# Performance work log

Measured on AMD Instinct MI355X. Metric: run time of the kernel, lower is better.

Reference implementation:

```python
import jax, jax.numpy as jnp
import numpy as np

SUPPORT = 10
NEIGHBOR_NUM = 20
DEGREE = 8
NEG_SLOPE = 0.2
EPS = 1e-12


def _norm(x, axis):
    n = jnp.linalg.norm(x, axis=axis, keepdims=True)
    return x / jnp.maximum(n, EPS)


def knn_index(v, k):
    # v: (b, n, 3) -> (b, n, k) indices of k nearest (self excluded)
    inner = jnp.einsum('bnd,bmd->bnm', v, v)
    quad = jnp.sum(v * v, axis=2)
    dist = quad[:, :, None] - 2.0 * inner + quad[:, None, :]
    _, idx = jax.lax.top_k(-dist, k + 1)  # smallest distances
    return idx[:, :, 1:]


def gather_nb(feat, idx):
    # feat (b,n,c), idx (b,n,k) -> (b,n,k,c)
    b = feat.shape[0]
    return feat[jnp.arange(b)[:, None, None], idx]


def nb_dir_norm(vertices, idx):
    nb = gather_nb(vertices, idx) - vertices[:, :, None, :]
    return _norm(nb, axis=-1)


def op3d(idx, vertices, directions, kernel_num):
    # Conv_surface: directions (3, support*kernel)
    ndn = nb_dir_norm(vertices, idx)                 # (b,n,k,3)
    sdn = _norm(directions, axis=0)
    theta = jax.nn.relu(jnp.einsum('bnkd,de->bnke', ndn, sdn))
    b, n, kk, _ = theta.shape
    theta = theta.reshape(b, n, kk, SUPPORT, kernel_num)
    return jnp.sum(jnp.max(theta, axis=2), axis=2)    # (b,n,kernel)


def opnd(idx, vertices, feat, w, bias, directions, out_ch):
    # Conv_layer: w (in,(s+1)*out), bias ((s+1)*out), directions (3, s*out)
    ndn = nb_dir_norm(vertices, idx)
    sdn = _norm(directions, axis=0)
    theta = jax.nn.relu(jnp.einsum('bnkd,de->bnke', ndn, sdn))  # (b,n,k,s*out)
    fo = feat @ w + bias                                        # (b,n,(s+1)*out)
    fc = fo[:, :, :out_ch]
    fs = gather_nb(fo[:, :, out_ch:], idx)                      # (b,n,k,s*out)
    b, n, kk, _ = theta.shape
    act = (theta * fs).reshape(b, n, kk, SUPPORT, out_ch)
    return fc + jnp.sum(jnp.max(act, axis=2), axis=2)


def tree_gcn(x, w_root, w_branch, w_l1, w_l2, bias, activation):
    # depth-0 upsampling TreeGCN: x (b,node,in) -> (b,node*DEGREE,out)
    b, node, in_f = x.shape
    root = x @ w_root                                           # (b,node,out)
    br = jax.nn.leaky_relu(jnp.einsum('bni,nij->bnj', x, w_branch), NEG_SLOPE)
    br = br.reshape(b, node * DEGREE, in_f)
    br = (br @ w_l1) @ w_l2                                     # (b,node*deg,out)
    out = jnp.repeat(root, DEGREE, axis=1) + br
    if activation:
        out = jax.nn.leaky_relu(out + jnp.tile(bias, (1, node, 1)), NEG_SLOPE)
    return out


def setup_inputs() -> dict:
    key = jax.random.key(0)
    ks = iter(jax.random.split(key, 32))
    r = lambda shape: (jax.random.normal(next(ks), shape, dtype=jnp.float32) * 0.1)
    inp = {
        'coase_points': jax.random.normal(next(ks), (2, 512, 3), dtype=jnp.float32),
        'd0': r((3, SUPPORT * 32)),
        'w1': r((32, (SUPPORT + 1) * 64)), 'b1': r(((SUPPORT + 1) * 64,)), 'dir1': r((3, SUPPORT * 64)),
        'd2': r((3, SUPPORT * 32)),
        'w3': r((32, (SUPPORT + 1) * 64)), 'b3': r(((SUPPORT + 1) * 64,)), 'dir3': r((3, SUPPORT * 64)),
        'w4': r((64, (SUPPORT + 1) * 64)), 'b4': r(((SUPPORT + 1) * 64,)), 'dir4': r((3, SUPPORT * 64)),
        'w5': r((64, (SUPPORT + 1) * 64)), 'b5': r(((SUPPORT + 1) * 64,)), 'dir5': r((3, SUPPORT * 64)),
        'root1': r((64, 3)), 'branch1': r((512, 64, DEGREE * 64)),
        'loop1a': r((64, 64 * SUPPORT)), 'loop1b': r((64 * SUPPORT, 3)), 'bias1': r((1, DEGREE, 3)),
        'root2': r((64, 3)), 'branch2': r((4096, 64, DEGREE * 64)),
        'loop2a': r((64, 64 * SUPPORT)), 'loop2b': r((64 * SUPPORT, 3)),
    }
    return inp


def reference(coase_points, d0, w1, b1, dir1, d2, w3, b3, dir3, w4, b4, dir4,
              w5, b5, dir5, root1, branch1, loop1a, loop1b, bias1,
              root2, branch2, loop2a, loop2b):
    idx = knn_index(coase_points, NEIGHBOR_NUM)
    fm0 = jax.nn.relu(op3d(idx, coase_points, d0, 32))  # dropout is identity in eval
    fm1 = jax.nn.relu(opnd(idx, coase_points, fm0, w1, b1, dir1, 64))
    pc1 = tree_gcn(fm1, root1, branch1, loop1a, loop1b, bias1, True)   # (b, 4096, 3)
    idx2 = knn_index(pc1, NEIGHBOR_NUM)
    fm2 = jax.nn.relu(op3d(idx2, pc1, d2, 32))
    fm3 = jax.nn.relu(opnd(idx2, pc1, fm2, w3, b3, dir3, 64))
    fm4 = jax.nn.relu(opnd(idx2, pc1, fm3, w4, b4, dir4, 64))
    fm5 = jax.nn.relu(opnd(idx2, pc1, fm4, w5, b5, dir5, 64))
    pc2 = tree_gcn(fm5, root2, branch2, loop2a, loop2b, None, False)   # (b, 32768, 3)
    return pc1, pc2
```

## Files before the change

kernel.cpp:

```cpp
#include <hip/hip_runtime.h>
#include <hip/hip_bf16.h>
#include <stdint.h>

#define SUPPORT 10
#define KNN 20
#define DEGREE 8

__global__ __launch_bounds__(256) void prep_kernel(
    const float* __restrict__ d0, const float* __restrict__ dir1,
    const float* __restrict__ d2, const float* __restrict__ dir3,
    const float* __restrict__ dir4, const float* __restrict__ dir5,
    float* __restrict__ sdn0, float* __restrict__ sdn1, float* __restrict__ sdn2,
    float* __restrict__ sdn3, float* __restrict__ sdn4, float* __restrict__ sdn5,
    const float* __restrict__ l1a, const float* __restrict__ l1b,
    const float* __restrict__ l2a, const float* __restrict__ l2b,
    float* __restrict__ wc1, float* __restrict__ wc2,
    const float* __restrict__ pts1,
    float* __restrict__ px1, float* __restrict__ py1, float* __restrict__ pz1) {
#pragma clang fp contract(off)
  if (blockIdx.x < 13) {
    int t = blockIdx.x * 256 + threadIdx.x;
    if (t >= 3200) return;
    const float* src; float* dst; int cols; int e;
    if (t < 320)       { src = d0;   dst = sdn0; cols = 320; e = t; }
    else if (t < 960)  { src = dir1; dst = sdn1; cols = 640; e = t - 320; }
    else if (t < 1280) { src = d2;   dst = sdn2; cols = 320; e = t - 960; }
    else if (t < 1920) { src = dir3; dst = sdn3; cols = 640; e = t - 1280; }
    else if (t < 2560) { src = dir4; dst = sdn4; cols = 640; e = t - 1920; }
    else               { src = dir5; dst = sdn5; cols = 640; e = t - 2560; }
    float a = src[e], b = src[cols + e], c = src[2 * cols + e];
    float nrm = sqrtf(a * a + b * b + c * c);
    nrm = fmaxf(nrm, 1e-12f);
    dst[e] = a / nrm; dst[cols + e] = b / nrm; dst[2 * cols + e] = c / nrm;
  } else if (blockIdx.x < 15) {
    int which = blockIdx.x - 13;
    int tt = threadIdx.x;
    if (tt >= 192) return;
    const float* A  = which ? l2a : l1a;
    const float* Bm = which ? l2b : l1b;
    float* out = which ? wc2 : wc1;
    int i = tt / 3, c = tt % 3;
    float s = 0.f;
    for (int k = 0; k < 640; ++k) s = fmaf(A[i * 640 + k], Bm[k * 3 + c], s);
    out[i * 3 + c] = s;
  } else {
    int t = (blockIdx.x - 15) * 256 + threadIdx.x;
    if (t >= 1024) return;
    px1[t] = pts1[t * 3];
    py1[t] = pts1[t * 3 + 1];
    pz1[t] = pts1[t * 3 + 2];
  }
}

template <int MPER, int WAVES>
__global__ __launch_bounds__(WAVES * 64) void knn_kernel(
    const float* __restrict__ px, const float* __restrict__ py,
    const float* __restrict__ pz, int N, int* __restrict__ idx_out,
    float* __restrict__ ndn) {
#pragma clang fp contract(off)
  extern __shared__ uint32_t kbuf[];
  int w = threadIdx.x >> 6, lane = threadIdx.x & 63;
  int g = blockIdx.x * WAVES + w;
  int b = g / N, n = g % N;
  volatile uint32_t* K = kbuf + (size_t)w * 64 * MPER;
  const float* PX = px + (size_t)b * N;
  const float* PY = py + (size_t)b * N;
  const float* PZ = pz + (size_t)b * N;

  float nx = PX[n], ny = PY[n], nz = PZ[n];
  float qn = nx * nx + ny * ny + nz * nz;

  unsigned long long mymin = ~0ull;
  for (int j = 0; j < MPER; ++j) {
    int m = j * 64 + lane;
    float mx = PX[m], my = PY[m], mz = PZ[m];
    float inner = nx * mx + ny * my + nz * mz;
    float qm = mx * mx + my * my + mz * mz;
    float d = (qn - 2.0f * inner) + qm;
    uint32_t u = __float_as_uint(d);
    u ^= (u & 0x80000000u) ? 0xFFFFFFFFu : 0x80000000u;
    K[lane * MPER + (j ^ (lane & (MPER - 1)))] = u;
    unsigned long long key = ((unsigned long long)u << 32) | (unsigned)m;
    mymin = key < mymin ? key : mymin;
  }
  unsigned pick = 0;
  for (int r = 0; r < 21; ++r) {
    unsigned long long best = mymin;
#pragma unroll
    for (int s = 1; s < 64; s <<= 1) {
      unsigned long long o = __shfl_xor(best, s, 64);
      best = o < best ? o : best;
    }
    unsigned m = (unsigned)best;
    if (r > 0 && lane == r - 1) pick = m;
    if (r == 20) break;
    int owner = m & 63, slot = m >> 6;
    if (lane == slot) K[owner * MPER + (slot ^ (owner & (MPER - 1)))] = 0xFFFFFFFFu;
    unsigned long long cand = ~0ull;
    if (lane < MPER) {
      uint32_t v = K[owner * MPER + (lane ^ (owner & (MPER - 1)))];
      cand = ((unsigned long long)v << 32) | (unsigned)(lane * 64 + owner);
    }
#pragma unroll
    for (int s = 1; s < 64; s <<= 1) {
      unsigned long long o = __shfl_xor(cand, s, 64);
      cand = o < cand ? o : cand;
    }
    if (lane == owner) mymin = cand;
  }
  if (lane < KNN) {
    idx_out[(size_t)g * KNN + lane] = (int)pick;
    float mx = PX[pick], my = PY[pick], mz = PZ[pick];
    float dx = mx - nx, dy = my - ny, dz = mz - nz;
    float nr = sqrtf(dx * dx + dy * dy + dz * dz);
    nr = fmaxf(nr, 1e-12f);
    size_t base = (size_t)g * 60 + (size_t)lane * 3;
    ndn[base] = dx / nr; ndn[base + 1] = dy / nr; ndn[base + 2] = dz / nr;
  }
}

__global__ __launch_bounds__(256) void op3dfo_kernel(const float* __restrict__ ndn,
                                                     const float* __restrict__ sdn,
                                                     const float* __restrict__ wmat,
                                                     const float* __restrict__ bias,
                                                     float* __restrict__ fo, int N) {
#pragma clang fp contract(off)
  __shared__ float ndL[8 * 60];
  __shared__ float fL[8 * 32];
  int t = threadIdx.x;
  int gbase = blockIdx.x * 8;
  for (int i = t; i < 8 * 60; i += 256) ndL[i] = ndn[(size_t)gbase * 60 + i];
  __syncthreads();
  {
    int gg = t >> 5, c = t & 31;
    const float* nd = ndL + gg * 60;
    float sv0[SUPPORT], sv1[SUPPORT], sv2[SUPPORT], mm[SUPPORT];
#pragma unroll
    for (int s = 0; s < SUPPORT; ++s) {
      sv0[s] = sdn[s * 32 + c];
      sv1[s] = sdn[320 + s * 32 + c];
      sv2[s] = sdn[640 + s * 32 + c];
      mm[s] = 0.f;
    }
    for (int k = 0; k < KNN; ++k) {
      float nx = nd[k * 3], ny = nd[k * 3 + 1], nz = nd[k * 3 + 2];
#pragma unroll
      for (int s = 0; s < SUPPORT; ++s) {
        float th = nx * sv0[s] + ny * sv1[s] + nz * sv2[s];
        mm[s] = fmaxf(mm[s], th);
      }
    }
    float acc = 0.f;
#pragma unroll
    for (int s = 0; s < SUPPORT; ++s) acc += mm[s];
    fL[gg * 32 + c] = acc;
  }
  __syncthreads();
  float a0[8], a1[8], a2[8];
#pragma unroll
  for (int gg = 0; gg < 8; ++gg) { a0[gg] = 0.f; a1[gg] = 0.f; a2[gg] = 0.f; }
  bool has3 = (t < 192);
  for (int i = 0; i < 32; ++i) {
    float w0 = wmat[i * 704 + t];
    float w1 = wmat[i * 704 + t + 256];
    float w2 = has3 ? wmat[i * 704 + t + 512] : 0.f;
#pragma unroll
    for (int gg = 0; gg < 8; ++gg) {
      float f = fL[gg * 32 + i];
      a0[gg] = fmaf(f, w0, a0[gg]);
      a1[gg] = fmaf(f, w1, a1[gg]);
      a2[gg] = fmaf(f, w2, a2[gg]);
    }
  }
  float b0 = bias[t], b1 = bias[t + 256], b2 = has3 ? bias[t + 512] : 0.f;
#pragma unroll
  for (int gg = 0; gg < 8; ++gg) {
    size_t base = (size_t)(gbase + gg) * 704;
    fo[base + t] = a0[gg] + b0;
    fo[base + t + 256] = a1[gg] + b1;
    if (has3) fo[base + t + 512] = a2[gg] + b2;
  }
}

__global__ __launch_bounds__(256) void fo_kernel(const float* __restrict__ feat,
                                                 const float* __restrict__ wmat,
                                                 const float* __restrict__ bias,
                                                 float* __restrict__ fo, int N) {
  __shared__ float fL[8 * 64];
  int t = threadIdx.x;
  int gbase = blockIdx.x * 8;
  for (int i = t; i < 8 * 64; i += 256) fL[i] = feat[(size_t)gbase * 64 + i];
  __syncthreads();
  float a0[8], a1[8], a2[8];
#pragma unroll
  for (int gg = 0; gg < 8; ++gg) { a0[gg] = 0.f; a1[gg] = 0.f; a2[gg] = 0.f; }
  bool has3 = (t < 192);
  for (int i = 0; i < 64; ++i) {
    float w0 = wmat[i * 704 + t];
    float w1 = wmat[i * 704 + t + 256];
    float w2 = has3 ? wmat[i * 704 + t + 512] : 0.f;
#pragma unroll
    for (int gg = 0; gg < 8; ++gg) {
      float f = fL[gg * 64 + i];
      a0[gg] = fmaf(f, w0, a0[gg]);
      a1[gg] = fmaf(f, w1, a1[gg]);
      a2[gg] = fmaf(f, w2, a2[gg]);
    }
  }
  float b0 = bias[t], b1 = bias[t + 256], b2 = has3 ? bias[t + 512] : 0.f;
#pragma unroll
  for (int gg = 0; gg < 8; ++gg) {
    size_t base = (size_t)(gbase + gg) * 704;
    fo[base + t] = a0[gg] + b0;
    fo[base + t + 256] = a1[gg] + b1;
    if (has3) fo[base + t + 512] = a2[gg] + b2;
  }
}

__global__ __launch_bounds__(256) void opnd_kernel(const float* __restrict__ ndn,
                                                   const int* __restrict__ idx,
                                                   const float* __restrict__ fo,
                                                   const float* __restrict__ sdn,
                                                   float* __restrict__ fm, int N) {
#pragma clang fp contract(off)
  __shared__ float ndL[4][64];
  __shared__ int offL[4][24];
  int nb = gridDim.x;
  int lb = (blockIdx.x & 7) * (nb >> 3) + (blockIdx.x >> 3);
  int w = threadIdx.x >> 6, lane = threadIdx.x & 63;
  int g = lb * 4 + w;
  if (lane < 60) ndL[w][lane] = ndn[(size_t)g * 60 + lane];
  if (lane < KNN) offL[w][lane] = ((g / N) * N + idx[(size_t)g * KNN + lane]) * 704 + 64;
  __syncthreads();
  const float* ndw = ndL[w];
  const int* offw = offL[w];
  float sv0[SUPPORT], sv1[SUPPORT], sv2[SUPPORT], mm[SUPPORT];
#pragma unroll
  for (int s = 0; s < SUPPORT; ++s) {
    sv0[s] = sdn[s * 64 + lane];
    sv1[s] = sdn[640 + s * 64 + lane];
    sv2[s] = sdn[1280 + s * 64 + lane];
    mm[s] = -__builtin_inff();
  }
  for (int k = 0; k < KNN; ++k) {
    float nx = ndw[k * 3], ny = ndw[k * 3 + 1], nz = ndw[k * 3 + 2];
    int off = offw[k];
#pragma unroll
    for (int s = 0; s < SUPPORT; ++s) {
      float t = fmaxf(nx * sv0[s] + ny * sv1[s] + nz * sv2[s], 0.f);
      float f = fo[(size_t)off + s * 64 + lane];
      mm[s] = fmaxf(mm[s], t * f);
    }
  }
  float acc = 0.f;
#pragma unroll
  for (int s = 0; s < SUPPORT; ++s) acc += mm[s];
  float fc = fo[(size_t)g * 704 + lane];
  float v = fc + acc;
  fm[(size_t)g * 64 + lane] = fmaxf(v, 0.f);
}

__global__ __launch_bounds__(256) void tree_exact_kernel(
    const float* __restrict__ x, const float* __restrict__ wroot,
    const float* __restrict__ wb, const float* __restrict__ l1,
    const float* __restrict__ l2, const float* __restrict__ bias,
    float* __restrict__ out, int node,
    float* __restrict__ px2, float* __restrict__ py2, float* __restrict__ pz2) {
#pragma clang fp contract(off)
  __shared__ float xL[2][64];
  __shared__ float brL[2][512];
  __shared__ float tL[16][640];
  __shared__ float rootv[2][3];
  int n = blockIdx.x, t = threadIdx.x;
  if (t < 128) xL[t >> 6][t & 63] = x[(size_t)(t >> 6) * node * 64 + (size_t)n * 64 + (t & 63)];
  __syncthreads();
  {
    const float* wrow = wb + (size_t)n * 64 * 512;
    int j0 = 2 * t;
    float a00 = 0.f, a01 = 0.f, a10 = 0.f, a11 = 0.f;
    for (int i = 0; i < 64; ++i) {
      float w0 = wrow[(size_t)i * 512 + j0];
      float w1 = wrow[(size_t)i * 512 + j0 + 1];
      float f0 = xL[0][i], f1 = xL[1][i];
      a00 = a00 + f0 * w0; a01 = a01 + f0 * w1;
      a10 = a10 + f1 * w0; a11 = a11 + f1 * w1;
    }
    brL[0][j0]     = a00 >= 0.f ? a00 : 0.2f * a00;
    brL[0][j0 + 1] = a01 >= 0.f ? a01 : 0.2f * a01;
    brL[1][j0]     = a10 >= 0.f ? a10 : 0.2f * a10;
    brL[1][j0 + 1] = a11 >= 0.f ? a11 : 0.2f * a11;
  }
  if (t < 6) {
    int b = t / 3, c = t % 3;
    float r = 0.f;
    for (int i = 0; i < 64; ++i) r = fmaf(xL[b][i], wroot[i * 3 + c], r);
    rootv[b][c] = r;
  }
  __syncthreads();
#pragma unroll 4
  for (int u = 0; u < 40; ++u) {
    int e = u * 256 + t;
    int p = e / 640, j = e % 640;
    const float* brow = brL[p >> 3] + (p & 7) * 64;
    float acc = 0.f;
    for (int i = 0; i < 64; ++i)
      acc = fmaf(brow[i], l1[i * 640 + j], acc);
    tL[p][j] = acc;
  }
  __syncthreads();
  if (t < 48) {
    int p = t / 3, c = t % 3, b = p >> 3, d = p & 7;
    float s = 0.f;
    for (int j = 0; j < 640; ++j) s = fmaf(tL[p][j], l2[j * 3 + c], s);
    float v = rootv[b][c] + s;
    v = v + bias[d * 3 + c];
    v = v >= 0.f ? v : 0.2f * v;
    out[((size_t)b * node * DEGREE + (size_t)n * DEGREE + d) * 3 + c] = v;
    int p2 = b * node * DEGREE + n * DEGREE + d;
    if (c == 0) px2[p2] = v; else if (c == 1) py2[p2] = v; else pz2[p2] = v;
  }
}

__global__ __launch_bounds__(256) void tree_kernel(const float* __restrict__ x,
                                                   const float* __restrict__ wroot,
                                                   const float* __restrict__ wb,
                                                   const float* __restrict__ wc,
                                                   float* __restrict__ out,
                                                   int node) {
  __shared__ float xL[2][2][64];
  __shared__ float brL[2][2][512];
  int t = threadIdx.x;
  int n0 = blockIdx.x * 2;
  {
    int which = t >> 6;
    int ns = which >> 1, bb = which & 1;
    xL[ns][bb][t & 63] = x[(size_t)bb * node * 64 + (size_t)(n0 + ns) * 64 + (t & 63)];
  }
  __syncthreads();
  int ns = t >> 7;
  int j0 = (t & 127) * 4;
  const float* wrow = wb + (size_t)(n0 + ns) * 64 * 512;
  float a0x = 0.f, a0y = 0.f, a0z = 0.f, a0w = 0.f;
  float a1x = 0.f, a1y = 0.f, a1z = 0.f, a1w = 0.f;
  for (int i = 0; i < 64; ++i) {
    float4 wv = *(const float4*)(wrow + (size_t)i * 512 + j0);
    float f0 = xL[ns][0][i], f1 = xL[ns][1][i];
    a0x += f0 * wv.x; a0y += f0 * wv.y; a0z += f0 * wv.z; a0w += f0 * wv.w;
    a1x += f1 * wv.x; a1y += f1 * wv.y; a1z += f1 * wv.z; a1w += f1 * wv.w;
  }
  brL[ns][0][j0]     = a0x >= 0.f ? a0x : 0.2f * a0x;
  brL[ns][0][j0 + 1] = a0y >= 0.f ? a0y : 0.2f * a0y;
  brL[ns][0][j0 + 2] = a0z >= 0.f ? a0z : 0.2f * a0z;
  brL[ns][0][j0 + 3] = a0w >= 0.f ? a0w : 0.2f * a0w;
  brL[ns][1][j0]     = a1x >= 0.f ? a1x : 0.2f * a1x;
  brL[ns][1][j0 + 1] = a1y >= 0.f ? a1y : 0.2f * a1y;
  brL[ns][1][j0 + 2] = a1z >= 0.f ? a1z : 0.2f * a1z;
  brL[ns][1][j0 + 3] = a1w >= 0.f ? a1w : 0.2f * a1w;
  __syncthreads();
  if (t < 96) {
    int nsub = t / 48, rem = t % 48;
    int b = rem / 24, r2 = rem % 24, d = r2 / 3, c = r2 % 3;
    float root = 0.f, brs = 0.f;
    for (int i = 0; i < 64; ++i) {
      root = fmaf(xL[nsub][b][i], wroot[i * 3 + c], root);
      brs  = fmaf(brL[nsub][b][d * 64 + i], wc[i * 3 + c], brs);
    }
    float v = root + brs;
    out[((size_t)b * node * DEGREE + (size_t)(n0 + nsub) * DEGREE + d) * 3 + c] = v;
  }
}

extern "C" void kernel_launch(void* const* d_in, const int* in_sizes, int n_in,
                              void* d_out, int out_size, void* d_ws, size_t ws_size,
                              hipStream_t stream) {
  const float* pts1    = (const float*)d_in[0];
  const float* d0      = (const float*)d_in[1];
  const float* w1      = (const float*)d_in[2];
  const float* b1      = (const float*)d_in[3];
  const float* dir1    = (const float*)d_in[4];
  const float* d2      = (const float*)d_in[5];
  const float* w3      = (const float*)d_in[6];
  const float* b3      = (const float*)d_in[7];
  const float* dir3    = (const float*)d_in[8];
  const float* w4      = (const float*)d_in[9];
  const float* b4      = (const float*)d_in[10];
  const float* dir4    = (const float*)d_in[11];
  const float* w5      = (const float*)d_in[12];
  const float* b5      = (const float*)d_in[13];
  const float* dir5    = (const float*)d_in[14];
  const float* root1   = (const float*)d_in[15];
  const float* branch1 = (const float*)d_in[16];
  const float* l1a     = (const float*)d_in[17];
  const float* l1b     = (const float*)d_in[18];
  const float* bias1   = (const float*)d_in[19];
  const float* root2   = (const float*)d_in[20];
  const float* branch2 = (const float*)d_in[21];
  const float* l2a     = (const float*)d_in[22];
  const float* l2b     = (const float*)d_in[23];

  float* ws = (float*)d_ws;
  size_t o = 0;
  float* sdn0 = ws + o; o += 960;
  float* sdn1 = ws + o; o += 1920;
  float* sdn2 = ws + o; o += 960;
  float* sdn3 = ws + o; o += 1920;
  float* sdn4 = ws + o; o += 1920;
  float* sdn5 = ws + o; o += 1920;
  float* wc1  = ws + o; o += 192;
  float* wc2  = ws + o; o += 192;
  float* px1  = ws + o; o += 1024;
  float* py1  = ws + o; o += 1024;
  float* pz1  = ws + o; o += 1024;
  float* px2  = ws + o; o += 8192;
  float* py2  = ws + o; o += 8192;
  float* pz2  = ws + o; o += 8192;
  int*   idxb = (int*)(ws + o); o += (size_t)2 * 4096 * KNN;
  float* ndnb = ws + o; o += (size_t)2 * 4096 * KNN * 3;
  float* fo   = ws + o; o += (size_t)2 * 4096 * 704;
  float* fmA  = ws + o; o += (size_t)2 * 4096 * 64;
  float* fmB  = ws + o; o += (size_t)2 * 4096 * 64;

  float* pc1 = (float*)d_out;
  float* pc2 = (float*)d_out + 2 * 4096 * 3;

  prep_kernel<<<19, 256, 0, stream>>>(d0, dir1, d2, dir3, dir4, dir5,
                                      sdn0, sdn1, sdn2, sdn3, sdn4, sdn5,
                                      l1a, l1b, l2a, l2b, wc1, wc2,
                                      pts1, px1, py1, pz1);

  knn_kernel<8, 4><<<2 * 512 / 4, 256, 4 * 64 * 8 * 4, stream>>>(px1, py1, pz1, 512, idxb, ndnb);
  op3dfo_kernel<<<2 * 512 / 8, 256, 0, stream>>>(ndnb, sdn0, w1, b1, fo, 512);
  opnd_kernel<<<2 * 512 / 4, 256, 0, stream>>>(ndnb, idxb, fo, sdn1, fmB, 512);
  tree_exact_kernel<<<512, 256, 0, stream>>>(fmB, root1, branch1, l1a, l1b,
                                             bias1, pc1, 512, px2, py2, pz2);

  knn_kernel<64, 2><<<2 * 4096 / 2, 128, 2 * 64 * 64 * 4, stream>>>(px2, py2, pz2, 4096, idxb, ndnb);
  op3dfo_kernel<<<2 * 4096 / 8, 256, 0, stream>>>(ndnb, sdn2, w3, b3, fo, 4096);
  opnd_kernel<<<2 * 4096 / 4, 256, 0, stream>>>(ndnb, idxb, fo, sdn3, fmB, 4096);
  fo_kernel<<<2 * 4096 / 8, 256, 0, stream>>>(fmB, w4, b4, fo, 4096);
  opnd_kernel<<<2 * 4096 / 4, 256, 0, stream>>>(ndnb, idxb, fo, sdn4, fmA, 4096);
  fo_kernel<<<2 * 4096 / 8, 256, 0, stream>>>(fmA, w5, b5, fo, 4096);
  opnd_kernel<<<2 * 4096 / 4, 256, 0, stream>>>(ndnb, idxb, fo, sdn5, fmB, 4096);
  tree_kernel<<<4096 / 2, 256, 0, stream>>>(fmB, root2, branch2, wc2, pc2, 4096);
}
```

Baseline: 638.5 us.

## Morton-sort second-level points to improve locality of the whole stage-2 pipeline

```diff
diff --git a/kernel.cpp b/kernel.cpp
--- a/kernel.cpp
+++ b/kernel.cpp
@@ -52,16 +52,76 @@
   }
 }
 
-template <int MPER, int WAVES>
+__device__ __forceinline__ unsigned spread3(unsigned v) {
+  v = (v | (v << 16)) & 0x030000FFu;
+  v = (v | (v << 8))  & 0x0300F00Fu;
+  v = (v | (v << 4))  & 0x030C30C3u;
+  v = (v | (v << 2))  & 0x09249249u;
+  return v;
+}
+
+__global__ __launch_bounds__(256) void sort_kernel(
+    const float* __restrict__ px2, const float* __restrict__ py2,
+    const float* __restrict__ pz2,
+    float* __restrict__ pxp, float* __restrict__ pyp, float* __restrict__ pzp,
+    uint16_t* __restrict__ orig16, uint16_t* __restrict__ inv16) {
+  __shared__ unsigned long long keys[512];
+  int b = blockIdx.x, t = threadIdx.x;
+  const float* PX = px2 + (size_t)b * 4096;
+  const float* PY = py2 + (size_t)b * 4096;
+  const float* PZ = pz2 + (size_t)b * 4096;
+  for (int q = t; q < 512; q += 256) {
+    float x = PX[q * 8], y = PY[q * 8], z = PZ[q * 8];
+    unsigned xi = (unsigned)fminf(1023.f, fmaxf(0.f, (x + 2.f) * 256.f));
+    unsigned yi = (unsigned)fminf(1023.f, fmaxf(0.f, (y + 2.f) * 256.f));
+    unsigned zi = (unsigned)fminf(1023.f, fmaxf(0.f, (z + 2.f) * 256.f));
+    unsigned long long mc = spread3(xi) | ((unsigned long long)spread3(yi) << 1) |
+                            ((unsigned long long)spread3(zi) << 2);
+    keys[q] = (mc << 16) | (unsigned)q;
+  }
+  __syncthreads();
+  for (int k = 2; k <= 512; k <<= 1) {
+    for (int j = k >> 1; j > 0; j >>= 1) {
+      for (int i = t; i < 512; i += 256) {
+        int ixj = i ^ j;
+        if (ixj > i) {
+          bool up = ((i & k) == 0);
+          unsigned long long a = keys[i], c = keys[ixj];
+          bool sw = up ? (a > c) : (a < c);
+          if (sw) { keys[i] = c; keys[ixj] = a; }
+        }
+      }
+      __syncthreads();
+    }
+  }
+  for (int e = t; e < 4096; e += 256) {
+    int pos = e >> 3, c = e & 7;
+    int q = (int)(keys[pos] & 0xFFFFu);
+    int src = q * 8 + c;
+    size_t B = (size_t)b * 4096;
+    pxp[B + e] = PX[src]; pyp[B + e] = PY[src]; pzp[B + e] = PZ[src];
+    orig16[B + e] = (uint16_t)src;
+    inv16[B + src] = (uint16_t)e;
+  }
+}
+
+template <int MPER, int WAVES, bool PERM>
 __global__ __launch_bounds__(WAVES * 64) void knn_kernel(
     const float* __restrict__ px, const float* __restrict__ py,
     const float* __restrict__ pz, int N, int* __restrict__ idx_out,
-    float* __restrict__ ndn) {
+    float* __restrict__ ndn, const uint16_t* __restrict__ orig) {
 #pragma clang fp contract(off)
   extern __shared__ uint32_t kbuf[];
+  __shared__ uint16_t origT[PERM ? (MPER * 64) : 1];
   int w = threadIdx.x >> 6, lane = threadIdx.x & 63;
   int g = blockIdx.x * WAVES + w;
   int b = g / N, n = g % N;
+  if (PERM) {
+    int bb = (blockIdx.x * WAVES) / N;
+    const uint16_t* src = orig + (size_t)bb * N;
+    for (int i = threadIdx.x; i < N; i += WAVES * 64) origT[i] = src[i];
+    __syncthreads();
+  }
   volatile uint32_t* K = kbuf + (size_t)w * 64 * MPER;
   const float* PX = px + (size_t)b * N;
   const float* PY = py + (size_t)b * N;
@@ -80,7 +140,8 @@
     uint32_t u = __float_as_uint(d);
     u ^= (u & 0x80000000u) ? 0xFFFFFFFFu : 0x80000000u;
     K[lane * MPER + (j ^ (lane & (MPER - 1)))] = u;
-    unsigned long long key = ((unsigned long long)u << 32) | (unsigned)m;
+    unsigned om = PERM ? (unsigned)origT[m] : (unsigned)m;
+    unsigned long long key = ((unsigned long long)u << 24) | (unsigned)((om << 12) | m);
     mymin = key < mymin ? key : mymin;
   }
   unsigned pick = 0;
@@ -91,7 +152,7 @@
       unsigned long long o = __shfl_xor(best, s, 64);
       best = o < best ? o : best;
     }
-    unsigned m = (unsigned)best;
+    unsigned m = (unsigned)best & 0xFFFu;
     if (r > 0 && lane == r - 1) pick = m;
     if (r == 20) break;
     int owner = m & 63, slot = m >> 6;
@@ -99,7 +160,9 @@
     unsigned long long cand = ~0ull;
     if (lane < MPER) {
       uint32_t v = K[owner * MPER + (lane ^ (owner & (MPER - 1)))];
-      cand = ((unsigned long long)v << 32) | (unsigned)(lane * 64 + owner);
+      int mc = lane * 64 + owner;
+      unsigned om = PERM ? (unsigned)origT[mc] : (unsigned)mc;
+      cand = ((unsigned long long)v << 24) | (unsigned)((om << 12) | mc);
     }
 #pragma unroll
     for (int s = 1; s < 64; s <<= 1) {
@@ -326,7 +389,8 @@
                                                    const float* __restrict__ wb,
                                                    const float* __restrict__ wc,
                                                    float* __restrict__ out,
-                                                   int node) {
+                                                   int node,
+                                                   const uint16_t* __restrict__ inv16) {
   __shared__ float xL[2][2][64];
   __shared__ float brL[2][2][512];
   int t = threadIdx.x;
@@ -334,7 +398,8 @@
   {
     int which = t >> 6;
     int ns = which >> 1, bb = which & 1;
-    xL[ns][bb][t & 63] = x[(size_t)bb * node * 64 + (size_t)(n0 + ns) * 64 + (t & 63)];
+    int stor = (int)inv16[(size_t)bb * node + (n0 + ns)];
+    xL[ns][bb][t & 63] = x[((size_t)bb * node + stor) * 64 + (t & 63)];
   }
   __syncthreads();
   int ns = t >> 7;
@@ -414,6 +479,11 @@
   float* px2  = ws + o; o += 8192;
   float* py2  = ws + o; o += 8192;
   float* pz2  = ws + o; o += 8192;
+  float* pxp  = ws + o; o += 8192;
+  float* pyp  = ws + o; o += 8192;
+  float* pzp  = ws + o; o += 8192;
+  uint16_t* orig16 = (uint16_t*)(ws + o); o += 4096;
+  uint16_t* inv16  = (uint16_t*)(ws + o); o += 4096;
   int*   idxb = (int*)(ws + o); o += (size_t)2 * 4096 * KNN;
   float* ndnb = ws + o; o += (size_t)2 * 4096 * KNN * 3;
   float* fo   = ws + o; o += (size_t)2 * 4096 * 704;
@@ -428,18 +498,21 @@
                                       l1a, l1b, l2a, l2b, wc1, wc2,
                                       pts1, px1, py1, pz1);
 
-  knn_kernel<8, 4><<<2 * 512 / 4, 256, 4 * 64 * 8 * 4, stream>>>(px1, py1, pz1, 512, idxb, ndnb);
+  knn_kernel<8, 4, false><<<2 * 512 / 4, 256, 4 * 64 * 8 * 4, stream>>>(
+      px1, py1, pz1, 512, idxb, ndnb, nullptr);
   op3dfo_kernel<<<2 * 512 / 8, 256, 0, stream>>>(ndnb, sdn0, w1, b1, fo, 512);
   opnd_kernel<<<2 * 512 / 4, 256, 0, stream>>>(ndnb, idxb, fo, sdn1, fmB, 512);
   tree_exact_kernel<<<512, 256, 0, stream>>>(fmB, root1, branch1, l1a, l1b,
                                              bias1, pc1, 512, px2, py2, pz2);
 
-  knn_kernel<64, 2><<<2 * 4096 / 2, 128, 2 * 64 * 64 * 4, stream>>>(px2, py2, pz2, 4096, idxb, ndnb);
+  sort_kernel<<<2, 256, 0, stream>>>(px2, py2, pz2, pxp, pyp, pzp, orig16, inv16);
+  knn_kernel<64, 2, true><<<2 * 4096 / 2, 128, 2 * 64 * 64 * 4, stream>>>(
+      pxp, pyp, pzp, 4096, idxb, ndnb, orig16);
   op3dfo_kernel<<<2 * 4096 / 8, 256, 0, stream>>>(ndnb, sdn2, w3, b3, fo, 4096);
   opnd_kernel<<<2 * 4096 / 4, 256, 0, stream>>>(ndnb, idxb, fo, sdn3, fmB, 4096);
   fo_kernel<<<2 * 4096 / 8, 256, 0, stream>>>(fmB, w4, b4, fo, 4096);
   opnd_kernel<<<2 * 4096 / 4, 256, 0, stream>>>(ndnb, idxb, fo, sdn4, fmA, 4096);
   fo_kernel<<<2 * 4096 / 8, 256, 0, stream>>>(fmA, w5, b5, fo, 4096);
   opnd_kernel<<<2 * 4096 / 4, 256, 0, stream>>>(ndnb, idxb, fo, sdn5, fmB, 4096);
-  tree_kernel<<<4096 / 2, 256, 0, stream>>>(fmB, root2, branch2, wc2, pc2, 4096);
-}
+  tree_kernel<<<4096 / 2, 256, 0, stream>>>(fmB, root2, branch2, wc2, pc2, 4096, inv16);
+}
```

Result: slower. 683.0 us (+7.0%).
